# Optimization experiments

Measured on AMD Instinct MI355X. Metric: run time of the kernel, lower is better.

## Reference

```python
import jax, jax.numpy as jnp
import numpy as np

N, E, G = 50000, 800000, 500
IN_DIM, EXTRA, HID, HEADS, NCLS = 128, 32, 64, 4, 1
NODE_FEAT2 = HID * HEADS  # 256, input to layer 2
FINAL = NODE_FEAT2 + EXTRA
NODES_PER_GRAPH = N // G  # 100


def gat_layer(h, W, a_l, a_r, b, src, dst, internal_relu):
    # DGL GATConv: fc -> per-head attn logits -> leaky_relu -> edge softmax (over dst) -> weighted sum
    feat = (h @ W).reshape(N, HEADS, HID)            # [N,H,D]
    el = jnp.sum(feat * a_l, axis=-1)                # [N,H]
    er = jnp.sum(feat * a_r, axis=-1)                # [N,H]
    e = jax.nn.leaky_relu(el[src] + er[dst], negative_slope=0.2)  # [E,H]
    m = jax.ops.segment_max(e, dst, num_segments=N)  # [N,H] (stable softmax)
    ex = jnp.exp(e - m[dst])
    denom = jax.ops.segment_sum(ex, dst, num_segments=N)
    alpha = ex / denom[dst]                          # [E,H]
    msg = feat[src] * alpha[:, :, None]              # [E,H,D]
    rst = jax.ops.segment_sum(msg, dst, num_segments=N) + b.reshape(1, HEADS, HID)
    if internal_relu:
        rst = jax.nn.relu(rst)
    return rst


def setup_inputs() -> dict:
    key = jax.random.key(0)
    ks = jax.random.split(key, 20)
    s = 0.05
    inp = {
        "x": jax.random.normal(ks[0], (N, IN_DIM), jnp.float32),
        "desc": jax.random.normal(ks[1], (G, EXTRA), jnp.float32),
        "src": jax.random.randint(ks[2], (E,), 0, N, jnp.int32),
        "dst": jax.random.randint(ks[3], (E,), 0, N, jnp.int32),
        "graph_id": (jnp.arange(N) // NODES_PER_GRAPH).astype(jnp.int32),
        # layer 1 params
        "W1": jax.random.normal(ks[4], (IN_DIM, HEADS * HID), jnp.float32) * s,
        "al1": jax.random.normal(ks[5], (HEADS, HID), jnp.float32) * s,
        "ar1": jax.random.normal(ks[6], (HEADS, HID), jnp.float32) * s,
        "b1": jnp.zeros((HEADS * HID,), jnp.float32),
        # layer 2 params
        "W2": jax.random.normal(ks[7], (NODE_FEAT2, HEADS * HID), jnp.float32) * s,
        "al2": jax.random.normal(ks[8], (HEADS, HID), jnp.float32) * s,
        "ar2": jax.random.normal(ks[9], (HEADS, HID), jnp.float32) * s,
        "b2": jnp.zeros((HEADS * HID,), jnp.float32),
        # MLP head (weights stored [in,out])
        "fc1_w": jax.random.normal(ks[10], (FINAL, HID), jnp.float32) * s,
        "fc1_b": jnp.zeros((HID,), jnp.float32),
        "fc2_w": jax.random.normal(ks[11], (HID, HID // 2), jnp.float32) * s,
        "fc2_b": jnp.zeros((HID // 2,), jnp.float32),
        "out_w": jax.random.normal(ks[12], (HID // 2, NCLS), jnp.float32) * s,
        "out_b": jnp.zeros((NCLS,), jnp.float32),
    }
    return inp


def reference(x, desc, src, dst, graph_id, W1, al1, ar1, b1, W2, al2, ar2, b2,
              fc1_w, fc1_b, fc2_w, fc2_b, out_w, out_b):
    h = gat_layer(x, W1, al1, ar1, b1, src, dst, internal_relu=True)
    h = jax.nn.relu(h.reshape(N, -1))                # flatten heads + outer relu (dropout=0)
    h = gat_layer(h, W2, al2, ar2, b2, src, dst, internal_relu=False)
    h = jax.nn.relu(h.reshape(N, -1))
    # dgl.mean_nodes over batched graph
    hg = jax.ops.segment_sum(h, graph_id, num_segments=G) / float(NODES_PER_GRAPH)  # [G, 256]
    combined = jnp.concatenate([hg, desc], axis=1)   # [G, 288]
    z = jax.nn.relu(combined @ fc1_w + fc1_b)
    z = jax.nn.relu(z @ fc2_w + fc2_b)
    return z @ out_w + out_b                          # [G, 1]
```

## Files before the change

### kernel.cpp

```cpp
#include <hip/hip_runtime.h>
#include <hip/hip_bf16.h>

#define N_NODES 50000
#define N_EDGES 800000
#define N_GRAPHS 500
#define IN_DIM 128
#define EXTRA 32
#define HID 64
#define HEADS 4
#define F2 256
#define NODES_PER_GRAPH 100
#define SCAN_BLOCKS ((N_NODES + 1023) / 1024)

typedef unsigned short u16;
typedef __attribute__((ext_vector_type(8))) short short8;
typedef __attribute__((ext_vector_type(4))) float floatx4;

__device__ __forceinline__ float bf2f(u16 u) {
    union { unsigned int i; float f; } v;
    v.i = ((unsigned int)u) << 16;
    return v.f;
}
__device__ __forceinline__ u16 f2b(float f) {
    __hip_bfloat16 h = __float2bfloat16(f);
    return *reinterpret_cast<u16*>(&h);
}

#define CNT_BLK 3125
#define CVT_BLK 6250
#define RP1_BLK 16
#define RP2_BLK 32
__global__ __launch_bounds__(256) void prep_kernel(const int* __restrict__ dst,
                                                   int* __restrict__ cnt,
                                                   const float* __restrict__ x,
                                                   u16* __restrict__ xb,
                                                   const float* __restrict__ W1,
                                                   u16* __restrict__ BF1,
                                                   const float* __restrict__ W2,
                                                   u16* __restrict__ BF2) {
    int b = blockIdx.x, t = threadIdx.x;
    if (b < CNT_BLK) {
        int e = b * 256 + t;
        if (e < N_EDGES) atomicAdd(&cnt[dst[e]], 1);
    } else if (b < CNT_BLK + CVT_BLK) {
        int i = (b - CNT_BLK) * 256 + t;
        float4 v = reinterpret_cast<const float4*>(x)[i];
        ushort4 o;
        o.x = f2b(v.x); o.y = f2b(v.y); o.z = f2b(v.z); o.w = f2b(v.w);
        reinterpret_cast<ushort4*>(xb)[i] = o;
    } else {
        const float* W;
        u16* BF;
        int chunk;
        if (b < CNT_BLK + CVT_BLK + RP1_BLK) {
            W = W1; BF = BF1; chunk = (b - CNT_BLK - CVT_BLK) * 4 + (t >> 6);
        } else {
            W = W2; BF = BF2; chunk = (b - CNT_BLK - CVT_BLK - RP1_BLK) * 4 + (t >> 6);
        }
        int l = t & 63;
        int kt = chunk >> 4, ct = chunk & 15;
        int col = ct * 16 + (l & 15);
        int k0 = kt * 32 + 8 * (l >> 4);
        u16* p = BF + (size_t)chunk * 512 + l * 8;
#pragma unroll
        for (int j = 0; j < 8; ++j) p[j] = f2b(W[(size_t)(k0 + j) * 256 + col]);
    }
}

__global__ __launch_bounds__(1024) void scan_block_kernel(const int* __restrict__ cnt,
                                                          int* __restrict__ part,
                                                          int* __restrict__ bsum) {
    __shared__ int buf[1024];
    int b = blockIdx.x, t = threadIdx.x;
    int i = b * 1024 + t;
    buf[t] = (i < N_NODES) ? cnt[i] : 0;
    __syncthreads();
    for (int d = 1; d < 1024; d <<= 1) {
        int add = (t >= d) ? buf[t - d] : 0;
        __syncthreads();
        buf[t] += add;
        __syncthreads();
    }
    if (i < N_NODES) part[i] = buf[t];
    if (t == 1023) bsum[b] = buf[t];
}

__global__ __launch_bounds__(1024) void scan_finalize_kernel(const int* __restrict__ part,
                                                             const int* __restrict__ bsum,
                                                             int* __restrict__ offs) {
    __shared__ int sbase;
    int t = threadIdx.x;
    if (t < 64) {
        int v = (t < blockIdx.x) ? bsum[t] : 0;
#pragma unroll
        for (int d = 32; d > 0; d >>= 1) v += __shfl_xor(v, d);
        if (t == 0) sbase = v;
    }
    __syncthreads();
    int i = blockIdx.x * 1024 + t;
    if (i < N_NODES) {
        offs[i + 1] = part[i] + sbase;
        if (i == 0) offs[0] = 0;
    }
}

__global__ void scatter_w_kernel(const int* __restrict__ src, const int* __restrict__ dst,
                                 const int* __restrict__ offs, int* __restrict__ fill,
                                 int* __restrict__ csr_src, int* __restrict__ pos_arr,
                                 const float* __restrict__ el, const float* __restrict__ er,
                                 float* __restrict__ w) {
    int e = blockIdx.x * blockDim.x + threadIdx.x;
    if (e >= N_EDGES) return;
    int s = src[e], d = dst[e];
    int pos = offs[d] + atomicAdd(&fill[d], 1);
    csr_src[pos] = s;
    pos_arr[e] = pos;
    float4 l = *reinterpret_cast<const float4*>(&el[s * 4]);
    float4 r = *reinterpret_cast<const float4*>(&er[d * 4]);
    float4 o; float v;
    v = l.x + r.x; v = (v > 0.f) ? v : 0.2f * v; o.x = __expf(v);
    v = l.y + r.y; v = (v > 0.f) ? v : 0.2f * v; o.y = __expf(v);
    v = l.z + r.z; v = (v > 0.f) ? v : 0.2f * v; o.z = __expf(v);
    v = l.w + r.w; v = (v > 0.f) ? v : 0.2f * v; o.w = __expf(v);
    *reinterpret_cast<float4*>(&w[(size_t)pos * 4]) = o;
}

__global__ void edge_w_kernel(const int* __restrict__ src, const int* __restrict__ dst,
                              const int* __restrict__ pos_arr,
                              const float* __restrict__ el, const float* __restrict__ er,
                              float* __restrict__ w) {
    int e = blockIdx.x * blockDim.x + threadIdx.x;
    if (e >= N_EDGES) return;
    int s = src[e], d = dst[e], p = pos_arr[e];
    float4 l = *reinterpret_cast<const float4*>(&el[s * 4]);
    float4 r = *reinterpret_cast<const float4*>(&er[d * 4]);
    float4 o; float v;
    v = l.x + r.x; v = (v > 0.f) ? v : 0.2f * v; o.x = __expf(v);
    v = l.y + r.y; v = (v > 0.f) ? v : 0.2f * v; o.y = __expf(v);
    v = l.z + r.z; v = (v > 0.f) ? v : 0.2f * v; o.z = __expf(v);
    v = l.w + r.w; v = (v > 0.f) ? v : 0.2f * v; o.w = __expf(v);
    *reinterpret_cast<float4*>(&w[(size_t)p * 4]) = o;
}

template <int K>
__global__ __launch_bounds__(256) void gemm_mfma_attn_kernel(const u16* __restrict__ A,
                                                             const u16* __restrict__ BF,
                                                             const float* __restrict__ al,
                                                             const float* __restrict__ ar,
                                                             u16* __restrict__ C,
                                                             float* __restrict__ el,
                                                             float* __restrict__ er, int M) {
    __shared__ u16 astage[64][68];
    __shared__ u16 bstage[16384];
    int t = threadIdx.x;
    int wave = t >> 6, lane = t & 63;
    int wc = wave;
    int l15 = lane & 15, kg = lane >> 4;
    int row0 = blockIdx.x * 64;

    floatx4 acc[4][4];
#pragma unroll
    for (int s = 0; s < 4; ++s)
#pragma unroll
        for (int c = 0; c < 4; ++c) acc[s][c] = (floatx4)0.0f;

    int arow_l = t >> 3;
    int akoff = (t & 7) * 8;

    for (int ks = 0; ks < K / 64; ++ks) {
        __syncthreads();
#pragma unroll
        for (int i = 0; i < 2; ++i) {
            int rl = arow_l + i * 32;
            int gr = row0 + rl; if (gr >= M) gr = M - 1;
            *reinterpret_cast<short8*>(&astage[rl][akoff]) =
                *reinterpret_cast<const short8*>(A + (size_t)gr * K + ks * 64 + akoff);
        }
        {
            const u16* bp = BF + (size_t)ks * 16384;
#pragma unroll
            for (int j = 0; j < 8; ++j) {
                int idx = (j * 256 + t) * 8;
                *reinterpret_cast<short8*>(&bstage[idx]) =
                    *reinterpret_cast<const short8*>(&bp[idx]);
            }
        }
        __syncthreads();
#pragma unroll
        for (int ktl = 0; ktl < 2; ++ktl) {
            short8 a[4], b[4];
#pragma unroll
            for (int s = 0; s < 4; ++s)
                a[s] = *reinterpret_cast<const short8*>(&astage[s * 16 + l15][ktl * 32 + kg * 8]);
#pragma unroll
            for (int c = 0; c < 4; ++c)
                b[c] = *reinterpret_cast<const short8*>(
                           &bstage[(ktl * 16 + wc * 4 + c) * 512 + lane * 8]);
#pragma unroll
            for (int s = 0; s < 4; ++s)
#pragma unroll
                for (int c = 0; c < 4; ++c)
                    acc[s][c] = __builtin_amdgcn_mfma_f32_16x16x32_bf16(a[s], b[c], acc[s][c], 0, 0, 0);
        }
    }

    int ct0 = wc * 4;
    floatx4 pls[4], prs[4];
#pragma unroll
    for (int s = 0; s < 4; ++s) { pls[s] = (floatx4)0.0f; prs[s] = (floatx4)0.0f; }
#pragma unroll
    for (int c = 0; c < 4; ++c) {
        float wl = al[(ct0 + c) * 16 + l15];
        float wrr = ar[(ct0 + c) * 16 + l15];
#pragma unroll
        for (int s = 0; s < 4; ++s) {
            pls[s] += acc[s][c] * wl;
            prs[s] += acc[s][c] * wrr;
        }
    }
#pragma unroll
    for (int off = 1; off < 16; off <<= 1) {
#pragma unroll
        for (int s = 0; s < 4; ++s)
#pragma unroll
            for (int j = 0; j < 4; ++j) {
                pls[s][j] += __shfl_xor(pls[s][j], off);
                prs[s][j] += __shfl_xor(prs[s][j], off);
            }
    }
    if (l15 == 0) {
#pragma unroll
        for (int s = 0; s < 4; ++s)
#pragma unroll
            for (int j = 0; j < 4; ++j) {
                int n = row0 + s * 16 + kg * 4 + j;
                if (n < M) { el[n * 4 + wc] = pls[s][j]; er[n * 4 + wc] = prs[s][j]; }
            }
    }

    __syncthreads();
    u16* cbuf = &astage[0][0] + wave * 1088;
#pragma unroll
    for (int s = 0; s < 4; ++s) {
#pragma unroll
        for (int c = 0; c < 4; ++c)
#pragma unroll
            for (int j = 0; j < 4; ++j)
                cbuf[(kg * 4 + j) * 68 + c * 16 + l15] = f2b(acc[s][c][j]);
#pragma unroll
        for (int it = 0; it < 2; ++it) {
            int r = (lane >> 3) + it * 8;
            int cg = lane & 7;
            int grow = row0 + s * 16 + r;
            if (grow < M) {
                short8 v = *reinterpret_cast<const short8*>(cbuf + r * 68 + cg * 8);
                *reinterpret_cast<short8*>(C + (size_t)grow * 256 + wc * 64 + cg * 8) = v;
            }
        }
    }
}

__global__ __launch_bounds__(256) void gather_kernel(const u16* __restrict__ feat,
                                                     const float* __restrict__ w,
                                                     const int* __restrict__ offs,
                                                     const int* __restrict__ csr_src,
                                                     const float* __restrict__ bias,
                                                     u16* __restrict__ outb) {
    int n = blockIdx.x * 4 + (threadIdx.x >> 6);
    if (n >= N_NODES) return;
    int lane = threadIdx.x & 63;
    int h = lane >> 4;
    const ushort4* feat4 = reinterpret_cast<const ushort4*>(feat);
    int s0 = offs[n], s1 = offs[n + 1];
    float4 acc = make_float4(0.f, 0.f, 0.f, 0.f);
    float den = 0.f;
    int i = s0;
    for (; i + 4 <= s1; i += 4) {
        int n0 = csr_src[i], n1 = csr_src[i + 1], n2 = csr_src[i + 2], n3 = csr_src[i + 3];
        float x0 = w[(size_t)(i + 0) * 4 + h];
        float x1 = w[(size_t)(i + 1) * 4 + h];
        float x2 = w[(size_t)(i + 2) * 4 + h];
        float x3 = w[(size_t)(i + 3) * 4 + h];
        ushort4 f0 = feat4[(size_t)n0 * 64 + lane];
        ushort4 f1 = feat4[(size_t)n1 * 64 + lane];
        ushort4 f2 = feat4[(size_t)n2 * 64 + lane];
        ushort4 f3 = feat4[(size_t)n3 * 64 + lane];
        acc.x = fmaf(x0, bf2f(f0.x), acc.x); acc.y = fmaf(x0, bf2f(f0.y), acc.y);
        acc.z = fmaf(x0, bf2f(f0.z), acc.z); acc.w = fmaf(x0, bf2f(f0.w), acc.w);
        acc.x = fmaf(x1, bf2f(f1.x), acc.x); acc.y = fmaf(x1, bf2f(f1.y), acc.y);
        acc.z = fmaf(x1, bf2f(f1.z), acc.z); acc.w = fmaf(x1, bf2f(f1.w), acc.w);
        acc.x = fmaf(x2, bf2f(f2.x), acc.x); acc.y = fmaf(x2, bf2f(f2.y), acc.y);
        acc.z = fmaf(x2, bf2f(f2.z), acc.z); acc.w = fmaf(x2, bf2f(f2.w), acc.w);
        acc.x = fmaf(x3, bf2f(f3.x), acc.x); acc.y = fmaf(x3, bf2f(f3.y), acc.y);
        acc.z = fmaf(x3, bf2f(f3.z), acc.z); acc.w = fmaf(x3, bf2f(f3.w), acc.w);
        den += (x0 + x1) + (x2 + x3);
    }
    for (; i < s1; ++i) {
        int s = csr_src[i];
        float x = w[(size_t)i * 4 + h];
        ushort4 f = feat4[(size_t)s * 64 + lane];
        acc.x = fmaf(x, bf2f(f.x), acc.x); acc.y = fmaf(x, bf2f(f.y), acc.y);
        acc.z = fmaf(x, bf2f(f.z), acc.z); acc.w = fmaf(x, bf2f(f.w), acc.w);
        den += x;
    }
    float inv = (s1 > s0) ? 1.f / den : 0.f;
    float4 bv = reinterpret_cast<const float4*>(bias)[lane];
    ushort4 o;
    o.x = f2b(fmaxf(fmaf(acc.x, inv, bv.x), 0.f));
    o.y = f2b(fmaxf(fmaf(acc.y, inv, bv.y), 0.f));
    o.z = f2b(fmaxf(fmaf(acc.z, inv, bv.z), 0.f));
    o.w = f2b(fmaxf(fmaf(acc.w, inv, bv.w), 0.f));
    reinterpret_cast<ushort4*>(outb)[(size_t)n * 64 + lane] = o;
}

__global__ __launch_bounds__(256) void head_kernel(const u16* __restrict__ h2,
                                                   const float* __restrict__ desc,
                                                   const float* __restrict__ fc1_w,
                                                   const float* __restrict__ fc1_b,
                                                   const float* __restrict__ fc2_w,
                                                   const float* __restrict__ fc2_b,
                                                   const float* __restrict__ out_w,
                                                   const float* __restrict__ out_b,
                                                   float* __restrict__ out) {
    __shared__ float comb[288];
    __shared__ float z1[64];
    __shared__ float z2[32];
    int g = blockIdx.x, t = threadIdx.x;
    const u16* base = h2 + (size_t)g * NODES_PER_GRAPH * 256;
    float s0 = 0.f, s1 = 0.f, s2 = 0.f, s3 = 0.f;
    for (int i = 0; i < NODES_PER_GRAPH; i += 4) {
        s0 += bf2f(base[(size_t)(i + 0) * 256 + t]);
        s1 += bf2f(base[(size_t)(i + 1) * 256 + t]);
        s2 += bf2f(base[(size_t)(i + 2) * 256 + t]);
        s3 += bf2f(base[(size_t)(i + 3) * 256 + t]);
    }
    comb[t] = ((s0 + s1) + (s2 + s3)) * (1.f / NODES_PER_GRAPH);
    if (t < EXTRA) comb[256 + t] = desc[g * EXTRA + t];
    __syncthreads();
    if (t < 64) {
        float a = fc1_b[t];
        for (int i = 0; i < 288; ++i) a += comb[i] * fc1_w[i * 64 + t];
        z1[t] = fmaxf(a, 0.f);
    }
    __syncthreads();
    if (t < 32) {
        float a = fc2_b[t];
        for (int i = 0; i < 64; ++i) a += z1[i] * fc2_w[i * 32 + t];
        z2[t] = fmaxf(a, 0.f);
    }
    __syncthreads();
    if (t == 0) {
        float a = out_b[0];
        for (int i = 0; i < 32; ++i) a += z2[i] * out_w[i];
        out[g] = a;
    }
}

extern "C" void kernel_launch(void* const* d_in, const int* in_sizes, int n_in,
                              void* d_out, int out_size, void* d_ws, size_t ws_size,
                              hipStream_t stream) {
    const float* x     = (const float*)d_in[0];
    const float* desc  = (const float*)d_in[1];
    const int*   src   = (const int*)d_in[2];
    const int*   dst   = (const int*)d_in[3];
    const float* W1    = (const float*)d_in[5];
    const float* al1   = (const float*)d_in[6];
    const float* ar1   = (const float*)d_in[7];
    const float* b1    = (const float*)d_in[8];
    const float* W2    = (const float*)d_in[9];
    const float* al2   = (const float*)d_in[10];
    const float* ar2   = (const float*)d_in[11];
    const float* b2    = (const float*)d_in[12];
    const float* fc1_w = (const float*)d_in[13];
    const float* fc1_b = (const float*)d_in[14];
    const float* fc2_w = (const float*)d_in[15];
    const float* fc2_b = (const float*)d_in[16];
    const float* out_w = (const float*)d_in[17];
    const float* out_b = (const float*)d_in[18];
    float* out = (float*)d_out;

    char* ws = (char*)d_ws;
    size_t off = 0;
    auto alloc = [&](size_t bytes) -> void* {
        void* p = ws + off;
        off = (off + bytes + 255) & ~(size_t)255;
        return p;
    };
    u16*   xb      = (u16*)alloc((size_t)N_NODES * IN_DIM * 2);
    u16*   featb   = (u16*)alloc((size_t)N_NODES * 256 * 2);
    u16*   h1b     = (u16*)alloc((size_t)N_NODES * 256 * 2);
    u16*   h2b     = (u16*)alloc((size_t)N_NODES * 256 * 2);
    u16*   BF1     = (u16*)alloc((size_t)IN_DIM * 256 * 2);
    u16*   BF2     = (u16*)alloc((size_t)F2 * 256 * 2);
    float* el      = (float*)alloc((size_t)N_NODES * 4 * 4);
    float* er      = (float*)alloc((size_t)N_NODES * 4 * 4);
    int*   offs    = (int*)alloc((size_t)(N_NODES + 1) * 4);
    int*   cntfill = (int*)alloc((size_t)2 * N_NODES * 4);
    int*   part    = (int*)alloc((size_t)N_NODES * 4);
    int*   bsum    = (int*)alloc(64 * 4);
    int*   csr_src = (int*)alloc((size_t)N_EDGES * 4);
    int*   pos_arr = (int*)alloc((size_t)N_EDGES * 4);
    float* wbuf    = (float*)alloc((size_t)N_EDGES * 4 * 4);
    int* cnt = cntfill, *fill = cntfill + N_NODES;

    hipMemsetAsync(cntfill, 0, (size_t)2 * N_NODES * 4, stream);
    prep_kernel<<<CNT_BLK + CVT_BLK + RP1_BLK + RP2_BLK, 256, 0, stream>>>(
        dst, cnt, x, xb, W1, BF1, W2, BF2);
    scan_block_kernel<<<SCAN_BLOCKS, 1024, 0, stream>>>(cnt, part, bsum);
    scan_finalize_kernel<<<SCAN_BLOCKS, 1024, 0, stream>>>(part, bsum, offs);

    int gb = (N_NODES + 63) / 64;
    int eb = (N_EDGES + 255) / 256;
    int ngb = (N_NODES + 3) / 4;
    gemm_mfma_attn_kernel<IN_DIM><<<gb, 256, 0, stream>>>(xb, BF1, al1, ar1, featb, el, er, N_NODES);
    scatter_w_kernel<<<eb, 256, 0, stream>>>(src, dst, offs, fill, csr_src, pos_arr,
                                             el, er, wbuf);
    gather_kernel<<<ngb, 256, 0, stream>>>(featb, wbuf, offs, csr_src, b1, h1b);
    gemm_mfma_attn_kernel<F2><<<gb, 256, 0, stream>>>(h1b, BF2, al2, ar2, featb, el, er, N_NODES);
    edge_w_kernel<<<eb, 256, 0, stream>>>(src, dst, pos_arr, el, er, wbuf);
    gather_kernel<<<ngb, 256, 0, stream>>>(featb, wbuf, offs, csr_src, b2, h2b);
    head_kernel<<<N_GRAPHS, 256, 0, stream>>>(h2b, desc, fc1_w, fc1_b, fc2_w, fc2_b,
                                              out_w, out_b, out);
}
```

Measured before the change: 289.3 us.

## Keep GEMM B operand in registers and stream A directly, dropping shared staging

Reworks the fused GEMM plus attention-logit kernel so each wave preloads its whole slice of the weight matrix into registers and loads A fragments straight from global memory, one 16-row tile at a time. This removes the LDS staging of A and B and the barriers around it, keeping only a small per-wave buffer for the output transpose. The cost is heavy register use (up to 8 K-tiles times 4 short8 per lane for K=256), which may lower occupancy. A rows are also read redundantly by all four waves through cache rather than once through shared memory.

```diff
diff --git a/kernel.cpp b/kernel.cpp
--- a/kernel.cpp
+++ b/kernel.cpp
@@ -150,111 +150,82 @@
                                                              u16* __restrict__ C,
                                                              float* __restrict__ el,
                                                              float* __restrict__ er, int M) {
-    __shared__ u16 astage[64][68];
-    __shared__ u16 bstage[16384];
+    const int NKT = K / 32;
+    __shared__ u16 cxpose[4][16 * 68];
     int t = threadIdx.x;
     int wave = t >> 6, lane = t & 63;
-    int wc = wave;
     int l15 = lane & 15, kg = lane >> 4;
-    int row0 = blockIdx.x * 64;
-
-    floatx4 acc[4][4];
-#pragma unroll
-    for (int s = 0; s < 4; ++s)
-#pragma unroll
-        for (int c = 0; c < 4; ++c) acc[s][c] = (floatx4)0.0f;
-
-    int arow_l = t >> 3;
-    int akoff = (t & 7) * 8;
-
-    for (int ks = 0; ks < K / 64; ++ks) {
-        __syncthreads();
-#pragma unroll
-        for (int i = 0; i < 2; ++i) {
-            int rl = arow_l + i * 32;
-            int gr = row0 + rl; if (gr >= M) gr = M - 1;
-            *reinterpret_cast<short8*>(&astage[rl][akoff]) =
-                *reinterpret_cast<const short8*>(A + (size_t)gr * K + ks * 64 + akoff);
-        }
-        {
-            const u16* bp = BF + (size_t)ks * 16384;
-#pragma unroll
-            for (int j = 0; j < 8; ++j) {
-                int idx = (j * 256 + t) * 8;
-                *reinterpret_cast<short8*>(&bstage[idx]) =
-                    *reinterpret_cast<const short8*>(&bp[idx]);
+    int h = wave;
+    int ct0 = h * 4;
+
+    short8 breg[NKT][4];
+#pragma unroll
+    for (int kt = 0; kt < NKT; ++kt)
+#pragma unroll
+        for (int c = 0; c < 4; ++c)
+            breg[kt][c] = *reinterpret_cast<const short8*>(
+                              BF + (size_t)(kt * 16 + ct0 + c) * 512 + lane * 8);
+
+    float alv[4], arv[4];
+#pragma unroll
+    for (int c = 0; c < 4; ++c) {
+        alv[c] = al[(ct0 + c) * 16 + l15];
+        arv[c] = ar[(ct0 + c) * 16 + l15];
+    }
+
+    u16* cbuf = cxpose[wave];
+    for (int rt = 0; rt < 4; ++rt) {
+        int row0 = blockIdx.x * 64 + rt * 16;
+        if (row0 >= M) break;
+        int arow = row0 + l15; if (arow >= M) arow = M - 1;
+        const u16* Ap = A + (size_t)arow * K + kg * 8;
+
+        floatx4 acc[4];
+#pragma unroll
+        for (int c = 0; c < 4; ++c) acc[c] = (floatx4)0.0f;
+#pragma unroll
+        for (int kt = 0; kt < NKT; ++kt) {
+            short8 a = *reinterpret_cast<const short8*>(Ap + kt * 32);
+#pragma unroll
+            for (int c = 0; c < 4; ++c)
+                acc[c] = __builtin_amdgcn_mfma_f32_16x16x32_bf16(a, breg[kt][c], acc[c], 0, 0, 0);
+        }
+
+        floatx4 pl = (floatx4)0.0f, pr = (floatx4)0.0f;
+#pragma unroll
+        for (int c = 0; c < 4; ++c) {
+            pl += acc[c] * alv[c];
+            pr += acc[c] * arv[c];
+        }
+#pragma unroll
+        for (int off = 1; off < 16; off <<= 1) {
+#pragma unroll
+            for (int j = 0; j < 4; ++j) {
+                pl[j] += __shfl_xor(pl[j], off);
+                pr[j] += __shfl_xor(pr[j], off);
             }
         }
-        __syncthreads();
-#pragma unroll
-        for (int ktl = 0; ktl < 2; ++ktl) {
-            short8 a[4], b[4];
-#pragma unroll
-            for (int s = 0; s < 4; ++s)
-                a[s] = *reinterpret_cast<const short8*>(&astage[s * 16 + l15][ktl * 32 + kg * 8]);
-#pragma unroll
-            for (int c = 0; c < 4; ++c)
-                b[c] = *reinterpret_cast<const short8*>(
-                           &bstage[(ktl * 16 + wc * 4 + c) * 512 + lane * 8]);
-#pragma unroll
-            for (int s = 0; s < 4; ++s)
-#pragma unroll
-                for (int c = 0; c < 4; ++c)
-                    acc[s][c] = __builtin_amdgcn_mfma_f32_16x16x32_bf16(a[s], b[c], acc[s][c], 0, 0, 0);
-        }
-    }
-
-    int ct0 = wc * 4;
-    floatx4 pls[4], prs[4];
-#pragma unroll
-    for (int s = 0; s < 4; ++s) { pls[s] = (floatx4)0.0f; prs[s] = (floatx4)0.0f; }
-#pragma unroll
-    for (int c = 0; c < 4; ++c) {
-        float wl = al[(ct0 + c) * 16 + l15];
-        float wrr = ar[(ct0 + c) * 16 + l15];
-#pragma unroll
-        for (int s = 0; s < 4; ++s) {
-            pls[s] += acc[s][c] * wl;
-            prs[s] += acc[s][c] * wrr;
-        }
-    }
-#pragma unroll
-    for (int off = 1; off < 16; off <<= 1) {
-#pragma unroll
-        for (int s = 0; s < 4; ++s)
+        if (l15 == 0) {
 #pragma unroll
             for (int j = 0; j < 4; ++j) {
-                pls[s][j] += __shfl_xor(pls[s][j], off);
-                prs[s][j] += __shfl_xor(prs[s][j], off);
+                int n = row0 + kg * 4 + j;
+                if (n < M) { el[n * 4 + h] = pl[j]; er[n * 4 + h] = pr[j]; }
             }
-    }
-    if (l15 == 0) {
-#pragma unroll
-        for (int s = 0; s < 4; ++s)
-#pragma unroll
-            for (int j = 0; j < 4; ++j) {
-                int n = row0 + s * 16 + kg * 4 + j;
-                if (n < M) { el[n * 4 + wc] = pls[s][j]; er[n * 4 + wc] = prs[s][j]; }
-            }
-    }
-
-    __syncthreads();
-    u16* cbuf = &astage[0][0] + wave * 1088;
-#pragma unroll
-    for (int s = 0; s < 4; ++s) {
+        }
+
 #pragma unroll
         for (int c = 0; c < 4; ++c)
 #pragma unroll
             for (int j = 0; j < 4; ++j)
-                cbuf[(kg * 4 + j) * 68 + c * 16 + l15] = f2b(acc[s][c][j]);
+                cbuf[(kg * 4 + j) * 68 + c * 16 + l15] = f2b(acc[c][j]);
 #pragma unroll
         for (int it = 0; it < 2; ++it) {
             int r = (lane >> 3) + it * 8;
             int cg = lane & 7;
-            int grow = row0 + s * 16 + r;
+            int grow = row0 + r;
             if (grow < M) {
                 short8 v = *reinterpret_cast<const short8*>(cbuf + r * 68 + cg * 8);
-                *reinterpret_cast<short8*>(C + (size_t)grow * 256 + wc * 64 + cg * 8) = v;
+                *reinterpret_cast<short8*>(C + (size_t)grow * 256 + h * 64 + cg * 8) = v;
             }
         }
     }
```

New measurement: 291.6 us. About the same (+0.8%).
